# Kernel optimization log

Measured on AMD Instinct MI355X. Metric: run time of the kernel, lower is better.

## Reference

```python
import jax, jax.numpy as jnp
import numpy as np

N_NODES = 131072
N_EDGES = 262144
N_GRAPHS = 4096
EMB = 300
N_LAYERS = 5
N_TASKS = 12
N_EXPERTS = 8
GATE_DIM = 300
NUM_ATOM_TYPE = 120
NUM_CHIRALITY = 3
NUM_BOND_TYPE = 6
NUM_BOND_DIR = 3


def setup_inputs() -> dict:
    key = jax.random.key(0)
    ks = jax.random.split(key, 24)
    x = jnp.stack([
        jax.random.randint(ks[0], (N_NODES,), 0, NUM_ATOM_TYPE),
        jax.random.randint(ks[1], (N_NODES,), 0, NUM_CHIRALITY),
    ], axis=1)
    edge_index = jax.random.randint(ks[2], (2, N_EDGES), 0, N_NODES)
    edge_attr = jnp.stack([
        jax.random.randint(ks[3], (N_EDGES,), 0, NUM_BOND_TYPE),
        jax.random.randint(ks[4], (N_EDGES,), 0, NUM_BOND_DIR),
    ], axis=1)
    batch = jnp.sort(jax.random.randint(ks[5], (N_NODES,), 0, N_GRAPHS))

    s = 0.05
    atom_emb1 = jax.random.normal(ks[6], (NUM_ATOM_TYPE, EMB)) * s
    atom_emb2 = jax.random.normal(ks[7], (NUM_CHIRALITY, EMB)) * s
    edge_emb1 = jax.random.normal(ks[8], (N_LAYERS, NUM_BOND_TYPE, EMB)) * s
    edge_emb2 = jax.random.normal(ks[9], (N_LAYERS, NUM_BOND_DIR, EMB)) * s
    mlp_w1 = jax.random.normal(ks[10], (N_LAYERS, EMB, 2 * EMB)) * s
    mlp_b1 = jnp.zeros((N_LAYERS, 2 * EMB))
    mlp_w2 = jax.random.normal(ks[11], (N_LAYERS, 2 * EMB, EMB)) * s
    mlp_b2 = jnp.zeros((N_LAYERS, EMB))
    bn_gamma = jnp.ones((N_LAYERS, EMB))
    bn_beta = jnp.zeros((N_LAYERS, EMB))
    gate_w1 = jax.random.normal(ks[12], (EMB, GATE_DIM)) * s
    gate_b1 = jnp.zeros((GATE_DIM,))
    gate_bn_g = jnp.ones((GATE_DIM,))
    gate_bn_b = jnp.zeros((GATE_DIM,))
    gate_w2 = jax.random.normal(ks[13], (GATE_DIM, GATE_DIM)) * s
    gate_b2 = jnp.zeros((GATE_DIM,))
    cluster = jax.random.normal(ks[14], (N_EXPERTS, GATE_DIM)) * s
    experts_w = jax.random.normal(ks[15], (EMB, N_TASKS * N_EXPERTS)) * s
    experts_b = jnp.zeros((N_TASKS * N_EXPERTS,))
    return dict(x=x, edge_index=edge_index, edge_attr=edge_attr, batch=batch,
                atom_emb1=atom_emb1, atom_emb2=atom_emb2,
                edge_emb1=edge_emb1, edge_emb2=edge_emb2,
                mlp_w1=mlp_w1, mlp_b1=mlp_b1, mlp_w2=mlp_w2, mlp_b2=mlp_b2,
                bn_gamma=bn_gamma, bn_beta=bn_beta,
                gate_w1=gate_w1, gate_b1=gate_b1,
                gate_bn_g=gate_bn_g, gate_bn_b=gate_bn_b,
                gate_w2=gate_w2, gate_b2=gate_b2,
                cluster=cluster, experts_w=experts_w, experts_b=experts_b)


def _batchnorm(h, g, b, eps=1e-5):
    mu = h.mean(axis=0)
    var = h.var(axis=0)
    return g * (h - mu) * jax.lax.rsqrt(var + eps) + b


def _forward(x, edge_index, edge_attr, batch,
             atom_emb1, atom_emb2, edge_emb1, edge_emb2,
             mlp_w1, mlp_b1, mlp_w2, mlp_b2, bn_gamma, bn_beta,
             gate_w1, gate_b1, gate_bn_g, gate_bn_b, gate_w2, gate_b2,
             cluster, experts_w, experts_b):
    n = x.shape[0]
    src, dst = edge_index[0], edge_index[1]
    ea0, ea1 = edge_attr[:, 0], edge_attr[:, 1]
    # node input embedding
    h = atom_emb1[x[:, 0]] + atom_emb2[x[:, 1]]  # [N, EMB]
    n_layers = mlp_w1.shape[0]
    for l in range(n_layers):
        ee = edge_emb1[l][ea0] + edge_emb2[l][ea1]  # [E, EMB]
        # self loops: attr = (bond_type=4, dir=0) for every node
        self_ee = edge_emb1[l][4] + edge_emb2[l][0]  # [EMB]
        agg = jax.ops.segment_sum(h[src] + ee, dst, num_segments=n)
        agg = agg + h + self_ee  # self-loop messages
        hid = jax.nn.relu(agg @ mlp_w1[l] + mlp_b1[l])
        h = hid @ mlp_w2[l] + mlp_b2[l]
        h = _batchnorm(h, bn_gamma[l], bn_beta[l])
        if l < n_layers - 1:
            h = jax.nn.relu(h)
    # graph pooling (JK='last')
    sums = jax.ops.segment_sum(h, batch, num_segments=N_GRAPHS)  # [B, EMB]
    counts = jax.ops.segment_sum(jnp.ones((n, 1), h.dtype), batch, num_segments=N_GRAPHS)
    gnn_out = sums / jnp.maximum(counts, 1.0)  # mean pool
    gate_input = sums  # global_add_pool
    # experts head: sum(gnn_out[:, :, None] * W, dim=1) + b == gnn_out @ W + b
    n_experts = cluster.shape[0]
    clf_logit = (gnn_out @ experts_w + experts_b).reshape(N_GRAPHS, -1, n_experts)
    # gate network
    zh = _batchnorm(gate_input @ gate_w1 + gate_b1, gate_bn_g, gate_bn_b)
    z = jax.nn.relu(zh) @ gate_w2 + gate_b2  # [B, GATE_DIM]
    # q: temperature-scaled softmax over cosine similarity to cluster centroids
    zn = z / jnp.maximum(jnp.linalg.norm(z, axis=1, keepdims=True), 1e-6)
    cn = cluster / jnp.maximum(jnp.linalg.norm(cluster, axis=1, keepdims=True), 1e-6)
    q = jax.nn.softmax(10.0 * (zn @ cn.T), axis=-1)  # T = 10
    return clf_logit, z, q


def reference(x, edge_index, edge_attr, batch,
              atom_emb1, atom_emb2, edge_emb1, edge_emb2,
              mlp_w1, mlp_b1, mlp_w2, mlp_b2, bn_gamma, bn_beta,
              gate_w1, gate_b1, gate_bn_g, gate_bn_b, gate_w2, gate_b2,
              cluster, experts_w, experts_b):
    return _forward(x, edge_index, edge_attr, batch,
                    atom_emb1, atom_emb2, edge_emb1, edge_emb2,
                    mlp_w1, mlp_b1, mlp_w2, mlp_b2, bn_gamma, bn_beta,
                    gate_w1, gate_b1, gate_bn_g, gate_bn_b, gate_w2, gate_b2,
                    cluster, experts_w, experts_b)
```

## Files before the change

### kernel.cpp

```cpp
#include <hip/hip_runtime.h>
#include <hip/hip_bf16.h>

typedef unsigned short u16;
typedef unsigned int u32;

#define NN 131072
#define NE 262144
#define NG 4096
#define EMB 300
#define HID 600
#define NL 5
#define NTNE 96
#define NEXP 8

#define W1T_ROWS 640
#define W1T_K    328
#define W2T_ROWS 384
#define W2T_K    648
#define EE_S     304

typedef __attribute__((ext_vector_type(8)))  short  s16x8;
typedef __attribute__((ext_vector_type(8)))  __bf16 b16x8;
typedef __attribute__((ext_vector_type(16))) float  f32x16;

static __device__ __forceinline__ float u2f(u16 u) {
    union { u32 i; float f; } w; w.i = ((u32)u) << 16; return w.f;
}
static __device__ __forceinline__ u16 f2u(float f) {
    union { float f; u32 i; } w; w.f = f;
    return (u16)((w.i + 0x7fffu + ((w.i >> 16) & 1u)) >> 16);
}

static __device__ __forceinline__ f32x16 mfma_3216(s16x8 a, s16x8 b, f32x16 c) {
    return __builtin_amdgcn_mfma_f32_32x32x16_bf16(
        __builtin_bit_cast(b16x8, a), __builtin_bit_cast(b16x8, b), c, 0, 0, 0);
}

__global__ void k_zero(float* __restrict__ p, int n) {
    int i = blockIdx.x * 256 + threadIdx.x;
    if (i < n) p[i] = 0.f;
}
__global__ void k_zero_int(int* __restrict__ p, int n) {
    int i = blockIdx.x * 256 + threadIdx.x;
    if (i < n) p[i] = 0;
}

__global__ void k_embed(const int* __restrict__ x, const float* __restrict__ ae1,
                        const float* __restrict__ ae2, u16* __restrict__ h) {
    int i = blockIdx.x;
    int a0 = x[2 * i], a1 = x[2 * i + 1];
    for (int f = threadIdx.x; f < EMB; f += blockDim.x)
        h[(size_t)i * EMB + f] = f2u(ae1[a0 * EMB + f] + ae2[a1 * EMB + f]);
}

__global__ void k_hist(const int* __restrict__ ei, int* __restrict__ deg) {
    int e = blockIdx.x * 256 + threadIdx.x;
    if (e < NE) atomicAdd(&deg[ei[NE + e]], 1);
}

__global__ __launch_bounds__(1024) void k_scan(const int* __restrict__ deg,
                                               int* __restrict__ rowstart) {
    __shared__ int lds[1024];
    int tid = threadIdx.x;
    int base = tid * 128;
    int s = 0;
    for (int j = 0; j < 128; ++j) s += deg[base + j];
    lds[tid] = s;
    __syncthreads();
    for (int off = 1; off < 1024; off <<= 1) {
        int v = (tid >= off) ? lds[tid - off] : 0;
        __syncthreads();
        lds[tid] += v;
        __syncthreads();
    }
    int run = (tid == 0) ? 0 : lds[tid - 1];
    for (int j = 0; j < 128; ++j) {
        rowstart[base + j] = run;
        run += deg[base + j];
    }
    if (tid == 1023) rowstart[NN] = run;
}

__global__ void k_fill(const int* __restrict__ ei, const int* __restrict__ ea,
                       int* __restrict__ deg, const int* __restrict__ rowstart,
                       u32* __restrict__ payload) {
    int e = blockIdx.x * 256 + threadIdx.x;
    if (e >= NE) return;
    int src = ei[e], dst = ei[NE + e];
    int c = ea[2 * e] * 3 + ea[2 * e + 1];
    int old = atomicSub(&deg[dst], 1);
    int pos = rowstart[dst] + old - 1;
    payload[pos] = (u32)src | ((u32)c << 17);
}

__global__ void k_prep_w1(const float* __restrict__ w1, u16* __restrict__ w1t) {
    int n = blockIdx.x;
    int l = blockIdx.y;
    size_t dst = ((size_t)l * W1T_ROWS + n) * W1T_K;
    for (int k = threadIdx.x; k < W1T_K; k += blockDim.x) {
        u16 v = 0;
        if (n < HID && k < EMB) v = f2u(w1[(size_t)l * EMB * HID + (size_t)k * HID + n]);
        w1t[dst + k] = v;
    }
}
__global__ void k_prep_w2(const float* __restrict__ w2, u16* __restrict__ w2t) {
    int n = blockIdx.x;
    int l = blockIdx.y;
    size_t dst = ((size_t)l * W2T_ROWS + n) * W2T_K;
    for (int k = threadIdx.x; k < W2T_K; k += blockDim.x) {
        u16 v = 0;
        if (n < EMB && k < HID) v = f2u(w2[(size_t)l * HID * EMB + (size_t)k * EMB + n]);
        w2t[dst + k] = v;
    }
}

__global__ void k_prep_ee(const float* __restrict__ ee1, const float* __restrict__ ee2,
                          u16* __restrict__ eeT) {
    int c = blockIdx.x;
    int l = blockIdx.y;
    size_t dst = ((size_t)l * 18 + c) * EE_S;
    const float* e1 = ee1 + (size_t)l * 6 * EMB + (c / 3) * EMB;
    const float* e2 = ee2 + (size_t)l * 3 * EMB + (c % 3) * EMB;
    for (int f = threadIdx.x; f < EE_S; f += blockDim.x)
        eeT[dst + f] = (f < EMB) ? f2u(e1[f] + e2[f]) : (u16)0;
}

__global__ void k_prep_bn(const float* __restrict__ stats, const float* __restrict__ bg,
                          const float* __restrict__ bb, float invM,
                          u16* __restrict__ scT, u16* __restrict__ shT) {
    int t = threadIdx.x;
    if (t >= EE_S) return;
    if (t < EMB) {
        float mu = stats[t] * invM;
        float var = stats[EMB + t] * invM - mu * mu;
        float sc = bg[t] * rsqrtf(var + 1e-5f);
        scT[t] = f2u(sc);
        shT[t] = f2u(bb[t] - mu * sc);
    } else {
        scT[t] = 0; shT[t] = 0;
    }
}

template <bool APPLY_BN>
__global__ __launch_bounds__(256) void k_layer1(const u16* __restrict__ h,
                                                const u32* __restrict__ payload,
                                                const int* __restrict__ rowstart,
                                                const u16* __restrict__ eeT,
                                                const u16* __restrict__ scT,
                                                const u16* __restrict__ shT,
                                                const u16* __restrict__ w1t,
                                                const float* __restrict__ b1,
                                                u16* __restrict__ hid) {
    __shared__ __align__(16) u16 A_s[32 * 328];
    int tid = threadIdx.x;
    int lane = tid & 63, wc = tid >> 6;
    int l31 = lane & 31, lhi = lane >> 5;
    size_t rowBase = (size_t)blockIdx.x * 32;

    for (int idx = tid; idx < 32 * 28; idx += 256)
        A_s[(idx / 28) * 328 + 300 + (idx % 28)] = 0;
    __syncthreads();

    for (int task = tid; task < 32 * 75; task += 256) {
        int r = task / 75, fc = task - r * 75;
        int f0 = fc * 4;
        int i = (int)rowBase + r;
        int beg = rowstart[i], end = rowstart[i + 1];
        float sc0 = 1.f, sc1 = 1.f, sc2 = 1.f, sc3 = 1.f;
        float sh0 = 0.f, sh1 = 0.f, sh2 = 0.f, sh3 = 0.f;
        if (APPLY_BN) {
            ushort4 scv = *(const ushort4*)&scT[f0];
            ushort4 shv = *(const ushort4*)&shT[f0];
            sc0 = u2f(scv.x); sc1 = u2f(scv.y); sc2 = u2f(scv.z); sc3 = u2f(scv.w);
            sh0 = u2f(shv.x); sh1 = u2f(shv.y); sh2 = u2f(shv.z); sh3 = u2f(shv.w);
        }
        ushort4 hv = *(const ushort4*)&h[(size_t)i * EMB + f0];
        ushort4 ev = *(const ushort4*)&eeT[12 * EE_S + f0];
        float a0 = u2f(hv.x), a1 = u2f(hv.y), a2 = u2f(hv.z), a3 = u2f(hv.w);
        if (APPLY_BN) {
            a0 = fmaxf(a0 * sc0 + sh0, 0.f);
            a1 = fmaxf(a1 * sc1 + sh1, 0.f);
            a2 = fmaxf(a2 * sc2 + sh2, 0.f);
            a3 = fmaxf(a3 * sc3 + sh3, 0.f);
        }
        float v0 = a0 + u2f(ev.x), v1 = a1 + u2f(ev.y);
        float v2 = a2 + u2f(ev.z), v3 = a3 + u2f(ev.w);
        for (int e = beg; e < end; ++e) {
            u32 p = payload[e];
            int src = p & 0x1FFFF;
            ushort4 sv = *(const ushort4*)&h[(size_t)src * EMB + f0];
            ushort4 ec = *(const ushort4*)&eeT[(size_t)(p >> 17) * EE_S + f0];
            float g0 = u2f(sv.x), g1 = u2f(sv.y), g2 = u2f(sv.z), g3 = u2f(sv.w);
            if (APPLY_BN) {
                g0 = fmaxf(g0 * sc0 + sh0, 0.f);
                g1 = fmaxf(g1 * sc1 + sh1, 0.f);
                g2 = fmaxf(g2 * sc2 + sh2, 0.f);
                g3 = fmaxf(g3 * sc3 + sh3, 0.f);
            }
            v0 += g0 + u2f(ec.x);
            v1 += g1 + u2f(ec.y);
            v2 += g2 + u2f(ec.z);
            v3 += g3 + u2f(ec.w);
        }
        short4 o;
        o.x = (short)f2u(v0); o.y = (short)f2u(v1);
        o.z = (short)f2u(v2); o.w = (short)f2u(v3);
        *(short4*)&A_s[r * 328 + f0] = o;
    }
    __syncthreads();

    s16x8 afr[20];
    int abase = l31 * 328 + lhi * 8;
#pragma unroll
    for (int s = 0; s < 20; ++s) afr[s] = *(const s16x8*)&A_s[abase + s * 16];

    for (int c5 = 0; c5 < 5; ++c5) {
        int col = c5 * 128 + wc * 32 + l31;
        const u16* bp = w1t + (size_t)col * W1T_K + lhi * 8;
        f32x16 acc = {};
#pragma unroll
        for (int s = 0; s < 20; ++s)
            acc = mfma_3216(afr[s], *(const s16x8*)&bp[s * 16], acc);
        if (col < HID) {
            float bias = b1[col];
#pragma unroll
            for (int r = 0; r < 16; ++r) {
                int row = (r & 3) + 8 * (r >> 2) + 4 * lhi;
                hid[(rowBase + row) * HID + col] =
                    f2u(fmaxf(acc[r] + bias, 0.f));
            }
        }
    }
}

__global__ __launch_bounds__(256) void k_gemm2(const u16* __restrict__ hid,
                                               const u16* __restrict__ w2t,
                                               const float* __restrict__ b2,
                                               u16* __restrict__ hout) {
    __shared__ __align__(16) u16 A_s[64 * 72];
    __shared__ __align__(16) u16 B_s[128 * 72];
    int tid = threadIdx.x;
    int lane = tid & 63, wid = tid >> 6;
    int wr = wid >> 1, wc = wid & 1;
    int l31 = lane & 31, lhi = lane >> 5;
    size_t rowBase = (size_t)blockIdx.y * 64;
    int cc = blockIdx.x * 128;

    f32x16 acc0 = {}, acc1 = {};
    int aoff = (wr * 32 + l31) * 72 + lhi * 8;
    int boff0 = (wc * 64 + l31) * 72 + lhi * 8;
    int boff1 = boff0 + 32 * 72;

    for (int sl = 0; sl < 10; ++sl) {
        int k0 = sl * 64;
        for (int idx = tid; idx < 512; idx += 256) {
            int m = idx >> 3, kv = idx & 7;
            int k = k0 + kv * 8;
            s16x8 v = {};
            if (k < HID) v = *(const s16x8*)&hid[(rowBase + m) * HID + k];
            *(s16x8*)&A_s[m * 72 + kv * 8] = v;
        }
        for (int idx = tid; idx < 1024; idx += 256) {
            int n = idx >> 3, kv = idx & 7;
            *(s16x8*)&B_s[n * 72 + kv * 8] =
                *(const s16x8*)&w2t[(size_t)(cc + n) * W2T_K + k0 + kv * 8];
        }
        __syncthreads();

        int smax = (sl < 9) ? 4 : 2;
        for (int s = 0; s < smax; ++s) {
            s16x8 a  = *(const s16x8*)&A_s[aoff + s * 16];
            s16x8 ba = *(const s16x8*)&B_s[boff0 + s * 16];
            s16x8 bb = *(const s16x8*)&B_s[boff1 + s * 16];
            acc0 = mfma_3216(a, ba, acc0);
            acc1 = mfma_3216(a, bb, acc1);
        }
        __syncthreads();
    }

    int colA = cc + wc * 64 + l31;
    int colB = colA + 32;
    if (colA < EMB) {
        float bias = b2[colA];
#pragma unroll
        for (int r = 0; r < 16; ++r) {
            int row = (r & 3) + 8 * (r >> 2) + 4 * lhi;
            hout[(rowBase + wr * 32 + row) * EMB + colA] = f2u(acc0[r] + bias);
        }
    }
    if (colB < EMB) {
        float bias = b2[colB];
#pragma unroll
        for (int r = 0; r < 16; ++r) {
            int row = (r & 3) + 8 * (r >> 2) + 4 * lhi;
            hout[(rowBase + wr * 32 + row) * EMB + colB] = f2u(acc1[r] + bias);
        }
    }
}

__global__ void k_bn_stats_h(const u16* __restrict__ X, float* __restrict__ stats) {
    int t = threadIdx.x;
    int half = t / 160;
    int pr = t - half * 160;
    if (pr >= 150) return;
    float s0 = 0.f, s1 = 0.f, q0 = 0.f, q1 = 0.f;
    for (int r = blockIdx.x * 2 + half; r < NN; r += 512) {
        u32 v = *(const u32*)&X[(size_t)r * EMB + pr * 2];
        float a = u2f((u16)(v & 0xffff));
        float b = u2f((u16)(v >> 16));
        s0 += a; s1 += b; q0 += a * a; q1 += b * b;
    }
    atomicAdd(&stats[2 * pr], s0);
    atomicAdd(&stats[2 * pr + 1], s1);
    atomicAdd(&stats[EMB + 2 * pr], q0);
    atomicAdd(&stats[EMB + 2 * pr + 1], q1);
}

template <bool RELU>
__global__ void k_bn_apply_h(u16* __restrict__ X, const float* __restrict__ stats,
                             const float* __restrict__ g, const float* __restrict__ b, float invM) {
    int r = blockIdx.x;
    for (int f = threadIdx.x; f < EMB; f += blockDim.x) {
        float mu = stats[f] * invM;
        float var = stats[EMB + f] * invM - mu * mu;
        float v = (u2f(X[(size_t)r * EMB + f]) - mu) * rsqrtf(var + 1e-5f) * g[f] + b[f];
        if (RELU) v = fmaxf(v, 0.f);
        X[(size_t)r * EMB + f] = f2u(v);
    }
}

__global__ void k_bn_stats_f(const float* __restrict__ X, int M, float* __restrict__ stats) {
    int f = threadIdx.x;
    if (f >= EMB) return;
    float s = 0.f, s2 = 0.f;
    for (int r = blockIdx.x; r < M; r += gridDim.x) {
        float v = X[(size_t)r * EMB + f];
        s += v;
        s2 += v * v;
    }
    atomicAdd(&stats[f], s);
    atomicAdd(&stats[EMB + f], s2);
}

template <bool RELU>
__global__ void k_bn_apply_f(float* __restrict__ X, const float* __restrict__ stats,
                             const float* __restrict__ g, const float* __restrict__ b, float invM) {
    int r = blockIdx.x;
    for (int f = threadIdx.x; f < EMB; f += blockDim.x) {
        float mu = stats[f] * invM;
        float var = stats[EMB + f] * invM - mu * mu;
        float v = (X[(size_t)r * EMB + f] - mu) * rsqrtf(var + 1e-5f) * g[f] + b[f];
        if (RELU) v = fmaxf(v, 0.f);
        X[(size_t)r * EMB + f] = v;
    }
}

template <bool RELU>
__global__ __launch_bounds__(256) void k_gemm(const float* __restrict__ A,
                                              const float* __restrict__ B,
                                              const float* __restrict__ bias,
                                              float* __restrict__ C, int M, int N, int K) {
    __shared__ __align__(16) float As[16][68];
    __shared__ __align__(16) float Bs[16][68];
    int tid = threadIdx.x;
    int tx = tid & 15, ty = tid >> 4;
    int rowBase = blockIdx.y * 64;
    int colBase = blockIdx.x * 64;
    float acc[4][4] = {};
    for (int k0 = 0; k0 < K; k0 += 16) {
        for (int idx = tid; idx < 1024; idx += 256) {
            int m = idx >> 4, k = idx & 15;
            int gk = k0 + k;
            As[k][m] = (gk < K) ? A[(size_t)(rowBase + m) * K + gk] : 0.f;
        }
        for (int idx = tid; idx < 1024; idx += 256) {
            int kk = idx >> 6, n = idx & 63;
            int gk = k0 + kk, gn = colBase + n;
            Bs[kk][n] = (gk < K && gn < N) ? B[(size_t)gk * N + gn] : 0.f;
        }
        __syncthreads();
#pragma unroll
        for (int k = 0; k < 16; ++k) {
            const float* ar = &As[k][ty * 4];
            const float* br = &Bs[k][tx * 4];
            float a[4], b[4];
#pragma unroll
            for (int i = 0; i < 4; ++i) a[i] = ar[i];
#pragma unroll
            for (int j = 0; j < 4; ++j) b[j] = br[j];
#pragma unroll
            for (int i = 0; i < 4; ++i)
#pragma unroll
                for (int j = 0; j < 4; ++j) acc[i][j] += a[i] * b[j];
        }
        __syncthreads();
    }
#pragma unroll
    for (int i = 0; i < 4; ++i) {
        int r = rowBase + ty * 4 + i;
#pragma unroll
        for (int j = 0; j < 4; ++j) {
            int c = colBase + tx * 4 + j;
            if (c < N && r < M) {
                float v = acc[i][j] + bias[c];
                if (RELU) v = fmaxf(v, 0.f);
                C[(size_t)r * N + c] = v;
            }
        }
    }
}

__global__ void k_pool(const u16* __restrict__ h, const int* __restrict__ batch,
                       float* __restrict__ sums, float* __restrict__ counts) {
    __shared__ int range[2];
    int g = blockIdx.x;
    int t = threadIdx.x;
    if (t < 2) {
        int target = g + t;
        int lo = 0, hi = NN;
        while (lo < hi) {
            int mid = (lo + hi) >> 1;
            if (batch[mid] < target) lo = mid + 1; else hi = mid;
        }
        range[t] = lo;
    }
    __syncthreads();
    int beg = range[0], end = range[1];
    if (t < EMB) {
        float s = 0.f;
        for (int r = beg; r < end; ++r) s += u2f(h[(size_t)r * EMB + t]);
        sums[(size_t)g * EMB + t] = s;
    }
    if (t == 0) counts[g] = (float)(end - beg);
}

__global__ void k_clf(const float* __restrict__ sums, const float* __restrict__ counts,
                      const float* __restrict__ ew, const float* __restrict__ eb,
                      float* __restrict__ out) {
    int gi = blockIdx.x;
    int t = threadIdx.x;
    if (t >= NTNE) return;
    float cnt = fmaxf(counts[gi], 1.f);
    float acc = 0.f;
    for (int k = 0; k < EMB; ++k) acc += sums[(size_t)gi * EMB + k] * ew[k * NTNE + t];
    out[(size_t)gi * NTNE + t] = acc / cnt + eb[t];
}

__global__ void k_cnorm(const float* __restrict__ cluster, float* __restrict__ cnorm) {
    int l = threadIdx.x;
    for (int e = 0; e < NEXP; ++e) {
        float s = 0.f;
        for (int f = l; f < EMB; f += 64) {
            float v = cluster[e * EMB + f];
            s += v * v;
        }
        for (int o = 32; o; o >>= 1) s += __shfl_xor(s, o);
        if (l == 0) cnorm[e] = sqrtf(s);
    }
}

__global__ void k_zout(const float* __restrict__ z, float* __restrict__ out) {
    int gi = blockIdx.x;
    for (int f = threadIdx.x; f < EMB; f += blockDim.x)
        out[(size_t)gi * EMB + f] = z[(size_t)gi * EMB + f];
}

__global__ void k_q(const float* __restrict__ z, const float* __restrict__ cluster,
                    const float* __restrict__ cnorm, float* __restrict__ qout) {
    int gi = blockIdx.x;
    int l = threadIdx.x;
    float s = 0.f;
    for (int f = l; f < EMB; f += 64) {
        float v = z[(size_t)gi * EMB + f];
        s += v * v;
    }
    for (int o = 32; o; o >>= 1) s += __shfl_xor(s, o);
    float zn = fmaxf(sqrtf(s), 1e-6f);
    float sc[NEXP];
#pragma unroll
    for (int e = 0; e < NEXP; ++e) {
        float d = 0.f;
        for (int f = l; f < EMB; f += 64) d += z[(size_t)gi * EMB + f] * cluster[e * EMB + f];
        for (int o = 32; o; o >>= 1) d += __shfl_xor(d, o);
        sc[e] = 10.f * d / (zn * fmaxf(cnorm[e], 1e-6f));
    }
    float mx = sc[0];
#pragma unroll
    for (int e = 1; e < NEXP; ++e) mx = fmaxf(mx, sc[e]);
    float se = 0.f;
#pragma unroll
    for (int e = 0; e < NEXP; ++e) {
        sc[e] = expf(sc[e] - mx);
        se += sc[e];
    }
    if (l < NEXP) qout[(size_t)gi * NEXP + l] = sc[l] / se;
}

extern "C" void kernel_launch(void* const* d_in, const int* in_sizes, int n_in,
                              void* d_out, int out_size, void* d_ws, size_t ws_size,
                              hipStream_t stream) {
    const int* x       = (const int*)d_in[0];
    const int* ei      = (const int*)d_in[1];
    const int* ea      = (const int*)d_in[2];
    const int* batch   = (const int*)d_in[3];
    const float* ae1   = (const float*)d_in[4];
    const float* ae2   = (const float*)d_in[5];
    const float* ee1   = (const float*)d_in[6];
    const float* ee2   = (const float*)d_in[7];
    const float* w1    = (const float*)d_in[8];
    const float* b1    = (const float*)d_in[9];
    const float* w2    = (const float*)d_in[10];
    const float* b2    = (const float*)d_in[11];
    const float* bng   = (const float*)d_in[12];
    const float* bnb   = (const float*)d_in[13];
    const float* gw1   = (const float*)d_in[14];
    const float* gb1   = (const float*)d_in[15];
    const float* gbng  = (const float*)d_in[16];
    const float* gbnb  = (const float*)d_in[17];
    const float* gw2   = (const float*)d_in[18];
    const float* gb2   = (const float*)d_in[19];
    const float* clus  = (const float*)d_in[20];
    const float* ew    = (const float*)d_in[21];
    const float* eb    = (const float*)d_in[22];

    char* wp = (char*)d_ws;
    u16* hbuf = (u16*)wp;                 wp += (size_t)NN * EMB * sizeof(u16);
    u16* hid = (u16*)wp;                  wp += (size_t)NN * HID * sizeof(u16);
    float* stats = (float*)wp;            wp += 2 * EMB * sizeof(float);
    u16* w1t = (u16*)wp;                  wp += (size_t)NL * W1T_ROWS * W1T_K * sizeof(u16);
    u16* w2t = (u16*)wp;                  wp += (size_t)NL * W2T_ROWS * W2T_K * sizeof(u16);
    u16* eeT = (u16*)wp;                  wp += (size_t)NL * 18 * EE_S * sizeof(u16);
    u16* scT = (u16*)wp;                  wp += EE_S * sizeof(u16);
    u16* shT = (u16*)wp;                  wp += EE_S * sizeof(u16);
    int* deg = (int*)wp;                  wp += (size_t)NN * sizeof(int);
    int* rowstart = (int*)wp;             wp += (size_t)(NN + 4) * sizeof(int);
    u32* payload = (u32*)wp;              wp += (size_t)NE * sizeof(u32);

    float* sums   = (float*)hid;
    float* counts = sums + (size_t)NG * EMB;
    float* zh     = counts + NG;
    float* zb     = zh + (size_t)NG * EMB;
    float* cnorm  = zb + (size_t)NG * EMB;

    float* out     = (float*)d_out;
    float* out_clf = out;
    float* out_z   = out + (size_t)NG * NTNE;
    float* out_q   = out_z + (size_t)NG * EMB;

    k_zero_int<<<NN / 256, 256, 0, stream>>>(deg, NN);
    k_hist<<<NE / 256, 256, 0, stream>>>(ei, deg);
    k_scan<<<1, 1024, 0, stream>>>(deg, rowstart);
    k_fill<<<NE / 256, 256, 0, stream>>>(ei, ea, deg, rowstart, payload);

    k_prep_w1<<<dim3(W1T_ROWS, NL), 64, 0, stream>>>(w1, w1t);
    k_prep_w2<<<dim3(W2T_ROWS, NL), 64, 0, stream>>>(w2, w2t);
    k_prep_ee<<<dim3(18, NL), 128, 0, stream>>>(ee1, ee2, eeT);
    k_embed<<<NN, 320, 0, stream>>>(x, ae1, ae2, hbuf);

    for (int l = 0; l < NL; ++l) {
        const u16* eeL = eeT + (size_t)l * 18 * EE_S;
        if (l == 0)
            k_layer1<false><<<NN / 32, 256, 0, stream>>>(
                hbuf, payload, rowstart, eeL, nullptr, nullptr,
                w1t + (size_t)l * W1T_ROWS * W1T_K, b1 + (size_t)l * HID, hid);
        else
            k_layer1<true><<<NN / 32, 256, 0, stream>>>(
                hbuf, payload, rowstart, eeL, scT, shT,
                w1t + (size_t)l * W1T_ROWS * W1T_K, b1 + (size_t)l * HID, hid);
        k_gemm2<<<dim3(3, NN / 64), 256, 0, stream>>>(hid, w2t + (size_t)l * W2T_ROWS * W2T_K,
                                                      b2 + (size_t)l * EMB, hbuf);
        k_zero<<<3, 256, 0, stream>>>(stats, 2 * EMB);
        k_bn_stats_h<<<256, 320, 0, stream>>>(hbuf, stats);
        if (l < NL - 1)
            k_prep_bn<<<1, 320, 0, stream>>>(stats, bng + (size_t)l * EMB,
                                             bnb + (size_t)l * EMB, 1.f / NN, scT, shT);
    }

    k_bn_apply_h<false><<<NN, 320, 0, stream>>>(hbuf, stats, bng + (size_t)(NL - 1) * EMB,
                                                bnb + (size_t)(NL - 1) * EMB, 1.f / NN);

    k_pool<<<NG, 320, 0, stream>>>(hbuf, batch, sums, counts);
    k_clf<<<NG, 128, 0, stream>>>(sums, counts, ew, eb, out_clf);

    k_gemm<false><<<dim3(5, NG / 64), 256, 0, stream>>>(sums, gw1, gb1, zh, NG, EMB, EMB);
    k_zero<<<3, 256, 0, stream>>>(stats, 2 * EMB);
    k_bn_stats_f<<<256, 320, 0, stream>>>(zh, NG, stats);
    k_bn_apply_f<true><<<NG, 320, 0, stream>>>(zh, stats, gbng, gbnb, 1.f / NG);
    k_gemm<false><<<dim3(5, NG / 64), 256, 0, stream>>>(zh, gw2, gb2, zb, NG, EMB, EMB);

    k_cnorm<<<1, 64, 0, stream>>>(clus, cnorm);
    k_zout<<<NG, 320, 0, stream>>>(zb, out_z);
    k_q<<<NG, 64, 0, stream>>>(zb, clus, cnorm, out_q);
}
```

Before: 3.055 ms.

## Parallelize edge aggregation per edge with LDS float atomics in layer1

Replaces per-destination-row serial edge loops with an edge-parallel scheme: each block first writes self-loop terms into an fp32 LDS tile, then threads process (edge, feature-chunk) tasks and atomically add messages into the destination row's LDS slot. The destination's local row index is packed into the CSR payload. The aim is to remove load imbalance and serial dependency chains caused by varying node degree, at the cost of LDS atomic traffic, a larger fp32 staging tile and a bf16 conversion when building the MFMA fragments. Float atomic ordering makes summation order nondeterministic.

New measurement: 4.592 ms. 50.3% more time.

```diff
diff --git a/kernel.cpp b/kernel.cpp
--- a/kernel.cpp
+++ b/kernel.cpp
@@ -18,6 +18,7 @@
 #define W2T_ROWS 384
 #define W2T_K    648
 #define EE_S     304
+#define AF_S     324
 
 typedef __attribute__((ext_vector_type(8)))  short  s16x8;
 typedef __attribute__((ext_vector_type(8)))  __bf16 b16x8;
@@ -90,7 +91,7 @@
     int c = ea[2 * e] * 3 + ea[2 * e + 1];
     int old = atomicSub(&deg[dst], 1);
     int pos = rowstart[dst] + old - 1;
-    payload[pos] = (u32)src | ((u32)c << 17);
+    payload[pos] = (u32)src | ((u32)c << 17) | ((u32)(dst & 31) << 22);
 }
 
 __global__ void k_prep_w1(const float* __restrict__ w1, u16* __restrict__ w1t) {
@@ -151,68 +152,81 @@
                                                 const u16* __restrict__ w1t,
                                                 const float* __restrict__ b1,
                                                 u16* __restrict__ hid) {
-    __shared__ __align__(16) u16 A_s[32 * 328];
+    __shared__ __align__(16) float Af[32 * AF_S];
+    __shared__ int rs_s[33];
     int tid = threadIdx.x;
     int lane = tid & 63, wc = tid >> 6;
     int l31 = lane & 31, lhi = lane >> 5;
     size_t rowBase = (size_t)blockIdx.x * 32;
 
-    for (int idx = tid; idx < 32 * 28; idx += 256)
-        A_s[(idx / 28) * 328 + 300 + (idx % 28)] = 0;
+    if (tid < 33) rs_s[tid] = rowstart[rowBase + tid];
+
+    for (int task = tid; task < 32 * 81; task += 256) {
+        int r = task / 81, q = task - r * 81;
+        int f0 = q * 4;
+        float v0 = 0.f, v1 = 0.f, v2 = 0.f, v3 = 0.f;
+        if (f0 < EMB) {
+            int i = (int)rowBase + r;
+            ushort4 hv = *(const ushort4*)&h[(size_t)i * EMB + f0];
+            ushort4 ev = *(const ushort4*)&eeT[12 * EE_S + f0];
+            float a0 = u2f(hv.x), a1 = u2f(hv.y), a2 = u2f(hv.z), a3 = u2f(hv.w);
+            if (APPLY_BN) {
+                ushort4 scv = *(const ushort4*)&scT[f0];
+                ushort4 shv = *(const ushort4*)&shT[f0];
+                a0 = fmaxf(a0 * u2f(scv.x) + u2f(shv.x), 0.f);
+                a1 = fmaxf(a1 * u2f(scv.y) + u2f(shv.y), 0.f);
+                a2 = fmaxf(a2 * u2f(scv.z) + u2f(shv.z), 0.f);
+                a3 = fmaxf(a3 * u2f(scv.w) + u2f(shv.w), 0.f);
+            }
+            v0 = a0 + u2f(ev.x); v1 = a1 + u2f(ev.y);
+            v2 = a2 + u2f(ev.z); v3 = a3 + u2f(ev.w);
+        }
+        float4 o = {v0, v1, v2, v3};
+        *(float4*)&Af[r * AF_S + f0] = o;
+    }
     __syncthreads();
 
-    for (int task = tid; task < 32 * 75; task += 256) {
-        int r = task / 75, fc = task - r * 75;
-        int f0 = fc * 4;
-        int i = (int)rowBase + r;
-        int beg = rowstart[i], end = rowstart[i + 1];
-        float sc0 = 1.f, sc1 = 1.f, sc2 = 1.f, sc3 = 1.f;
-        float sh0 = 0.f, sh1 = 0.f, sh2 = 0.f, sh3 = 0.f;
-        if (APPLY_BN) {
-            ushort4 scv = *(const ushort4*)&scT[f0];
-            ushort4 shv = *(const ushort4*)&shT[f0];
-            sc0 = u2f(scv.x); sc1 = u2f(scv.y); sc2 = u2f(scv.z); sc3 = u2f(scv.w);
-            sh0 = u2f(shv.x); sh1 = u2f(shv.y); sh2 = u2f(shv.z); sh3 = u2f(shv.w);
-        }
-        ushort4 hv = *(const ushort4*)&h[(size_t)i * EMB + f0];
-        ushort4 ev = *(const ushort4*)&eeT[12 * EE_S + f0];
-        float a0 = u2f(hv.x), a1 = u2f(hv.y), a2 = u2f(hv.z), a3 = u2f(hv.w);
-        if (APPLY_BN) {
-            a0 = fmaxf(a0 * sc0 + sh0, 0.f);
-            a1 = fmaxf(a1 * sc1 + sh1, 0.f);
-            a2 = fmaxf(a2 * sc2 + sh2, 0.f);
-            a3 = fmaxf(a3 * sc3 + sh3, 0.f);
-        }
-        float v0 = a0 + u2f(ev.x), v1 = a1 + u2f(ev.y);
-        float v2 = a2 + u2f(ev.z), v3 = a3 + u2f(ev.w);
-        for (int e = beg; e < end; ++e) {
-            u32 p = payload[e];
+    {
+        int eBeg = rs_s[0], eEnd = rs_s[32];
+        int nt = (eEnd - eBeg) * 75;
+        for (int task = tid; task < nt; task += 256) {
+            int ei75 = task / 75;
+            int fc = task - ei75 * 75;
+            int f0 = fc * 4;
+            u32 p = payload[eBeg + ei75];
             int src = p & 0x1FFFF;
+            int combo = (p >> 17) & 31;
+            int dl = (p >> 22) & 31;
             ushort4 sv = *(const ushort4*)&h[(size_t)src * EMB + f0];
-            ushort4 ec = *(const ushort4*)&eeT[(size_t)(p >> 17) * EE_S + f0];
+            ushort4 ec = *(const ushort4*)&eeT[(size_t)combo * EE_S + f0];
             float g0 = u2f(sv.x), g1 = u2f(sv.y), g2 = u2f(sv.z), g3 = u2f(sv.w);
             if (APPLY_BN) {
-                g0 = fmaxf(g0 * sc0 + sh0, 0.f);
-                g1 = fmaxf(g1 * sc1 + sh1, 0.f);
-                g2 = fmaxf(g2 * sc2 + sh2, 0.f);
-                g3 = fmaxf(g3 * sc3 + sh3, 0.f);
+                ushort4 scv = *(const ushort4*)&scT[f0];
+                ushort4 shv = *(const ushort4*)&shT[f0];
+                g0 = fmaxf(g0 * u2f(scv.x) + u2f(shv.x), 0.f);
+                g1 = fmaxf(g1 * u2f(scv.y) + u2f(shv.y), 0.f);
+                g2 = fmaxf(g2 * u2f(scv.z) + u2f(shv.z), 0.f);
+                g3 = fmaxf(g3 * u2f(scv.w) + u2f(shv.w), 0.f);
             }
-            v0 += g0 + u2f(ec.x);
-            v1 += g1 + u2f(ec.y);
-            v2 += g2 + u2f(ec.z);
-            v3 += g3 + u2f(ec.w);
-        }
-        short4 o;
-        o.x = (short)f2u(v0); o.y = (short)f2u(v1);
-        o.z = (short)f2u(v2); o.w = (short)f2u(v3);
-        *(short4*)&A_s[r * 328 + f0] = o;
+            float* ap = &Af[dl * AF_S + f0];
+            atomicAdd(&ap[0], g0 + u2f(ec.x));
+            atomicAdd(&ap[1], g1 + u2f(ec.y));
+            atomicAdd(&ap[2], g2 + u2f(ec.z));
+            atomicAdd(&ap[3], g3 + u2f(ec.w));
+        }
     }
     __syncthreads();
 
     s16x8 afr[20];
-    int abase = l31 * 328 + lhi * 8;
-#pragma unroll
-    for (int s = 0; s < 20; ++s) afr[s] = *(const s16x8*)&A_s[abase + s * 16];
+    int abase = l31 * AF_S + lhi * 8;
+#pragma unroll
+    for (int s = 0; s < 20; ++s) {
+        const float* ap = &Af[abase + s * 16];
+        s16x8 t;
+#pragma unroll
+        for (int j = 0; j < 8; ++j) t[j] = (short)f2u(ap[j]);
+        afr[s] = t;
+    }
 
     for (int c5 = 0; c5 < 5; ++c5) {
         int col = c5 * 128 + wc * 32 + l31;
```
